# Optimization experiments

Measured on AMD Instinct MI355X. Metric: run time of the kernel, lower is better.

## Reference

```python
import jax, jax.numpy as jnp
import numpy as np

# Config constants (match init_kwargs / config)
B = 16        # config.BATCH_SIZE
T = 2048      # config.TRAIN_LEN
C = 256       # input channels (input_shape[-1])
K = 8         # kernel_size
F = 256       # nb_filters
DIL = 4       # dilation_rate


def setup_inputs() -> dict:
    key = jax.random.key(0)
    k1, k2, k3 = jax.random.split(key, 3)
    inputs = jax.random.normal(k1, (B, T, C), dtype=jnp.float32)
    kernel = jax.random.normal(k2, (C, K, F), dtype=jnp.float32) * 0.05
    bias = jax.random.normal(k3, (F,), dtype=jnp.float32) * 0.05
    return {"inputs": inputs, "kernel": kernel, "bias": bias}


def reference(inputs, kernel, bias):
    # Original TF layer computes, per (b,t,k,f):
    #   raw[b,t,k,f] = sum_c (x[b,t,c] * kernel[c,k,f] + bias[f])
    #               = conv[b,t,k,f] + C * bias[f]
    # (bias is added BEFORE the reduce_sum over the channel axis, so it is
    #  scaled by C — we reproduce that quirk faithfully.)
    # Then each (t,k) slice is scatter-added to output time t + k*dilation
    # (the gather_nd + zero-pad construction in TF implements exactly this
    #  dilated transposed-conv scatter; non-matching positions gather zeros),
    # and finally the last T timesteps are kept.
    Bq, Tq, Cq = inputs.shape
    Kq, Fq = kernel.shape[1], kernel.shape[2]
    conv = jnp.einsum('btc,ckf->btkf', inputs, kernel) + jnp.asarray(Cq, inputs.dtype) * bias
    L = Tq + (Kq - 1) * DIL  # final_time_len
    # scatter positions: out[i + j*DIL] += conv[:, i, j, :]
    pos = (jnp.arange(Tq)[:, None] + DIL * jnp.arange(Kq)[None, :]).reshape(-1)  # (T*K,)
    out = jnp.zeros((Bq, L, Fq), dtype=conv.dtype)
    out = out.at[:, pos, :].add(conv.reshape(Bq, Tq * Kq, Fq))
    return out[:, -Tq:, :]
```

## Files before the change

### kernel.cpp

```cpp
#include <hip/hip_runtime.h>
#include <hip/hip_bf16.h>


#define B_    16
#define T_    2048
#define C_    256
#define KT    8
#define F_    256
#define SH    28
#define BT    64
#define ROWS  (BT + SH)
#define CHW   (ROWS * 64)

typedef __attribute__((ext_vector_type(8))) short short8;
typedef __attribute__((ext_vector_type(4))) float floatx4;

__global__ __launch_bounds__(256) void wprep_kernel(const float* __restrict__ W,
                                                    ushort* __restrict__ Wf) {
    const int tid  = threadIdx.x;
    const int fid  = blockIdx.x * 4 + (tid >> 6);
    const int lane = tid & 63;
    const int g    = fid & 15;
    const int S    = fid >> 4;
    const int kh   = S & 1, j = (S >> 1) & 7, cs = S >> 4;
    const int c0   = cs * 64 + kh * 32 + (lane >> 4) * 8;
    const int f    = g * 16 + (lane & 15);
    short8 pk;
    #pragma unroll
    for (int i = 0; i < 8; ++i) {
        __hip_bfloat16 h = __float2bfloat16(W[((c0 + i) * KT + j) * F_ + f]);
        pk[i] = *reinterpret_cast<const short*>(&h);
    }
    *reinterpret_cast<short8*>(Wf + (size_t)fid * 512 + lane * 8) = pk;
}

__device__ inline short8 cvt8(float4 a, float4 b) {
    float v[8] = {a.x, a.y, a.z, a.w, b.x, b.y, b.z, b.w};
    short8 r;
    #pragma unroll
    for (int i = 0; i < 8; ++i) {
        __hip_bfloat16 h = __float2bfloat16(v[i]);
        r[i] = *reinterpret_cast<const short*>(&h);
    }
    return r;
}

__global__ __launch_bounds__(256, 2) void deconv_kernel(
        const float* __restrict__ x, const ushort* __restrict__ Wf,
        const float* __restrict__ bias, float* __restrict__ out) {
    __shared__ ushort xs[2 * CHW];
    const int t0   = blockIdx.x * BT;
    const int b    = blockIdx.y;
    const int tid  = threadIdx.x;
    const int lane = tid & 63, wf = tid >> 6;
    const int l16  = lane & 15, q = lane >> 4;

    const int r0 = tid >> 3,         g0 = tid & 7;
    const int r1 = (tid + 256) >> 3, g1 = tid & 7;
    const int r2 = (tid + 512) >> 3, g2 = tid & 7;

    float4 A0, B0, A1, B1, A2, B2;

#define STAGE_LOAD(cs_) do {                                                   \
        const float4 z_ = make_float4(0.f, 0.f, 0.f, 0.f);                     \
        A2 = z_; B2 = z_;                                                      \
        {   const float4* p_ = reinterpret_cast<const float4*>(                \
                x + ((size_t)(b * T_ + t0 + r0) * C_ + (cs_) * 64 + g0 * 8));  \
            A0 = p_[0]; B0 = p_[1]; }                                          \
        {   const float4* p_ = reinterpret_cast<const float4*>(                \
                x + ((size_t)(b * T_ + t0 + r1) * C_ + (cs_) * 64 + g1 * 8));  \
            A1 = p_[0]; B1 = p_[1]; }                                          \
        if (tid < 224 && t0 + r2 < T_) {                                       \
            const float4* p_ = reinterpret_cast<const float4*>(                \
                x + ((size_t)(b * T_ + t0 + r2) * C_ + (cs_) * 64 + g2 * 8));  \
            A2 = p_[0]; B2 = p_[1]; } } while (0)

#define STAGE_WRITE(buf_) do {                                                 \
        ushort* d_ = xs + (buf_) * CHW;                                        \
        *reinterpret_cast<short8*>(d_ + r0 * 64 + ((g0 ^ (r0 & 7)) * 8)) =     \
            cvt8(A0, B0);                                                      \
        *reinterpret_cast<short8*>(d_ + r1 * 64 + ((g1 ^ (r1 & 7)) * 8)) =     \
            cvt8(A1, B1);                                                      \
        if (tid < 224)                                                         \
            *reinterpret_cast<short8*>(d_ + r2 * 64 + ((g2 ^ (r2 & 7)) * 8)) = \
                cvt8(A2, B2);                                                  \
        } while (0)

#define LOAD_A(buf_, s_, arr) do {                                             \
        const int j_ = (s_) >> 1, kh_ = (s_) & 1;                              \
        const int rb_ = SH - 4 * j_ + l16;                                     \
        _Pragma("unroll")                                                      \
        for (int mf = 0; mf < 4; ++mf) {                                       \
            const int row_ = rb_ + mf * 16;                                    \
            arr[mf] = *reinterpret_cast<const short8*>(                        \
                xs + (buf_) * CHW + row_ * 64 +                                \
                (((kh_ * 4 + q) ^ (row_ & 7)) * 8));                           \
        } } while (0)

#define LOAD_B(S_, arr) do {                                                   \
        const ushort* p_ = wbase + (size_t)(S_) * 8192;                        \
        _Pragma("unroll")                                                      \
        for (int nf = 0; nf < 4; ++nf)                                         \
            arr[nf] = *reinterpret_cast<const short8*>(p_ + nf * 512);         \
        } while (0)

#define DO_MFMA(aa, bb) do {                                                   \
        _Pragma("unroll")                                                      \
        for (int mf = 0; mf < 4; ++mf)                                         \
            _Pragma("unroll")                                                  \
            for (int nf = 0; nf < 4; ++nf)                                     \
                acc[mf][nf] = __builtin_amdgcn_mfma_f32_16x16x32_bf16(         \
                    aa[mf], bb[nf], acc[mf][nf], 0, 0, 0);                     \
        } while (0)

    const ushort* wbase = Wf + wf * 2048 + (size_t)lane * 8;

    float bf4[4];
    #pragma unroll
    for (int nf = 0; nf < 4; ++nf) bf4[nf] = bias[wf * 64 + nf * 16 + l16];

    floatx4 acc[4][4];
    #pragma unroll
    for (int mf = 0; mf < 4; ++mf)
        #pragma unroll
        for (int nf = 0; nf < 4; ++nf)
            acc[mf][nf] = (floatx4){0.f, 0.f, 0.f, 0.f};

    short8 aA[4], aB[4], bA[4], bB[4];

    STAGE_LOAD(0);
    LOAD_B(0, bA);
    LOAD_B(1, bB);
    STAGE_WRITE(0);
    __syncthreads();

    for (int cs = 0; cs < 4; ++cs) {
        const int buf = cs & 1;
        if (cs < 3) STAGE_LOAD(cs + 1);
        LOAD_A(buf, 0, aA);
        LOAD_A(buf, 1, aB);
        #pragma unroll
        for (int s = 0; s < 16; s += 2) {
            const int S = cs * 16 + s;
            __builtin_amdgcn_s_setprio(1);
            DO_MFMA(aA, bA);
            __builtin_amdgcn_s_setprio(0);
            if (s < 14) LOAD_A(buf, s + 2, aA);
            LOAD_B((S + 2) & 63, bA);
            __builtin_amdgcn_s_setprio(1);
            DO_MFMA(aB, bB);
            __builtin_amdgcn_s_setprio(0);
            if (s < 14) LOAD_A(buf, s + 3, aB);
            LOAD_B((S + 3) & 63, bB);
        }
        if (cs < 3) STAGE_WRITE(buf ^ 1);
        __syncthreads();
    }

    #pragma unroll
    for (int mf = 0; mf < 4; ++mf) {
        #pragma unroll
        for (int nf = 0; nf < 4; ++nf) {
            const int f = wf * 64 + nf * 16 + l16;
            #pragma unroll
            for (int r = 0; r < 4; ++r) {
                const int t = t0 + mf * 16 + q * 4 + r;
                const int jmin = (t < T_ - SH) ? 0 : (((t - (T_ - SH)) >> 2) + 1);
                out[(size_t)(b * T_ + t) * F_ + f] =
                    acc[mf][nf][r] + (float)(8 - jmin) * 256.0f * bf4[nf];
            }
        }
    }
#undef STAGE_LOAD
#undef STAGE_WRITE
#undef LOAD_A
#undef LOAD_B
#undef DO_MFMA
}

extern "C" void kernel_launch(void* const* d_in, const int* in_sizes, int n_in,
                              void* d_out, int out_size, void* d_ws, size_t ws_size,
                              hipStream_t stream) {
    const float* x    = (const float*)d_in[0];
    const float* W    = (const float*)d_in[1];
    const float* bias = (const float*)d_in[2];
    float* out = (float*)d_out;
    ushort* Wf = (ushort*)d_ws;

    wprep_kernel<<<256, 256, 0, stream>>>(W, Wf);
    dim3 grid(T_ / BT, B_);
    deconv_kernel<<<grid, 256, 0, stream>>>(x, Wf, bias, out);
}
```

Before: 44.50 us.

## Retile deconv: 256-row time tiles per block, warps split time, block owns 64 filters

The block tiling changes from 64 time rows × 256 filters (warps split filters) to 256 time rows × 64 filters (warps split time). The channel chunk shrinks to 32, giving 8 stages, and the weight prep layout is reordered to match. Each block now loads only one quarter of the weights, and the shared x tile carries the halo over 256 rows instead of 64, so less redundant x is staged. In exchange the same x tile is reloaded by 4 filter-tile blocks. The number of pipeline iterations and barriers doubles, and the grid keeps 512 blocks.

```diff
diff --git a/kernel.cpp b/kernel.cpp
--- a/kernel.cpp
+++ b/kernel.cpp
@@ -8,9 +8,12 @@
 #define KT    8
 #define F_    256
 #define SH    28
-#define BT    64
+#define BT    256
+#define FW    64
 #define ROWS  (BT + SH)
-#define CHW   (ROWS * 64)
+#define CH    32
+#define CHW   (ROWS * CH)
+#define NTASK (ROWS * 4)
 
 typedef __attribute__((ext_vector_type(8))) short short8;
 typedef __attribute__((ext_vector_type(4))) float floatx4;
@@ -22,8 +25,8 @@
     const int lane = tid & 63;
     const int g    = fid & 15;
     const int S    = fid >> 4;
-    const int kh   = S & 1, j = (S >> 1) & 7, cs = S >> 4;
-    const int c0   = cs * 64 + kh * 32 + (lane >> 4) * 8;
+    const int j    = S & 7, cs = S >> 3;
+    const int c0   = cs * 32 + (lane >> 4) * 8;
     const int f    = g * 16 + (lane & 15);
     short8 pk;
     #pragma unroll
@@ -49,52 +52,50 @@
         const float* __restrict__ x, const ushort* __restrict__ Wf,
         const float* __restrict__ bias, float* __restrict__ out) {
     __shared__ ushort xs[2 * CHW];
-    const int t0   = blockIdx.x * BT;
-    const int b    = blockIdx.y;
+    const int bid  = blockIdx.x;
+    const int ft   = bid >> 7;
+    const int tb   = bid & 127;
+    const int b    = tb >> 3;
+    const int t0   = (tb & 7) * BT;
     const int tid  = threadIdx.x;
-    const int lane = tid & 63, wf = tid >> 6;
+    const int lane = tid & 63, w = tid >> 6;
     const int l16  = lane & 15, q = lane >> 4;
 
-    const int r0 = tid >> 3,         g0 = tid & 7;
-    const int r1 = (tid + 256) >> 3, g1 = tid & 7;
-    const int r2 = (tid + 512) >> 3, g2 = tid & 7;
-
-    float4 A0, B0, A1, B1, A2, B2;
+    float4 SA[5], SB[5];
 
 #define STAGE_LOAD(cs_) do {                                                   \
-        const float4 z_ = make_float4(0.f, 0.f, 0.f, 0.f);                     \
-        A2 = z_; B2 = z_;                                                      \
-        {   const float4* p_ = reinterpret_cast<const float4*>(                \
-                x + ((size_t)(b * T_ + t0 + r0) * C_ + (cs_) * 64 + g0 * 8));  \
-            A0 = p_[0]; B0 = p_[1]; }                                          \
-        {   const float4* p_ = reinterpret_cast<const float4*>(                \
-                x + ((size_t)(b * T_ + t0 + r1) * C_ + (cs_) * 64 + g1 * 8));  \
-            A1 = p_[0]; B1 = p_[1]; }                                          \
-        if (tid < 224 && t0 + r2 < T_) {                                       \
-            const float4* p_ = reinterpret_cast<const float4*>(                \
-                x + ((size_t)(b * T_ + t0 + r2) * C_ + (cs_) * 64 + g2 * 8));  \
-            A2 = p_[0]; B2 = p_[1]; } } while (0)
+        _Pragma("unroll")                                                      \
+        for (int k = 0; k < 5; ++k) {                                          \
+            const int task = tid + k * 256;                                    \
+            const int row_ = task >> 2, g_ = task & 3;                         \
+            SA[k] = make_float4(0.f, 0.f, 0.f, 0.f);                           \
+            SB[k] = make_float4(0.f, 0.f, 0.f, 0.f);                           \
+            if (task < NTASK && t0 + row_ < T_) {                              \
+                const float4* p_ = reinterpret_cast<const float4*>(            \
+                    x + ((size_t)(b * T_ + t0 + row_) * C_ +                   \
+                         (cs_) * CH + g_ * 8));                                \
+                SA[k] = p_[0]; SB[k] = p_[1];                                  \
+            } } } while (0)
 
 #define STAGE_WRITE(buf_) do {                                                 \
         ushort* d_ = xs + (buf_) * CHW;                                        \
-        *reinterpret_cast<short8*>(d_ + r0 * 64 + ((g0 ^ (r0 & 7)) * 8)) =     \
-            cvt8(A0, B0);                                                      \
-        *reinterpret_cast<short8*>(d_ + r1 * 64 + ((g1 ^ (r1 & 7)) * 8)) =     \
-            cvt8(A1, B1);                                                      \
-        if (tid < 224)                                                         \
-            *reinterpret_cast<short8*>(d_ + r2 * 64 + ((g2 ^ (r2 & 7)) * 8)) = \
-                cvt8(A2, B2);                                                  \
-        } while (0)
+        _Pragma("unroll")                                                      \
+        for (int k = 0; k < 5; ++k) {                                          \
+            const int task = tid + k * 256;                                    \
+            const int row_ = task >> 2, g_ = task & 3;                         \
+            if (task < NTASK)                                                  \
+                *reinterpret_cast<short8*>(                                    \
+                    d_ + row_ * CH + ((g_ ^ (row_ & 3)) * 8)) =                \
+                    cvt8(SA[k], SB[k]);                                        \
+        } } while (0)
 
-#define LOAD_A(buf_, s_, arr) do {                                             \
-        const int j_ = (s_) >> 1, kh_ = (s_) & 1;                              \
-        const int rb_ = SH - 4 * j_ + l16;                                     \
+#define LOAD_A(buf_, j_, arr) do {                                             \
+        const int rb_ = SH - 4 * (j_) + w * 64 + l16;                          \
         _Pragma("unroll")                                                      \
         for (int mf = 0; mf < 4; ++mf) {                                       \
             const int row_ = rb_ + mf * 16;                                    \
             arr[mf] = *reinterpret_cast<const short8*>(                        \
-                xs + (buf_) * CHW + row_ * 64 +                                \
-                (((kh_ * 4 + q) ^ (row_ & 7)) * 8));                           \
+                xs + (buf_) * CHW + row_ * CH + ((q ^ (row_ & 3)) * 8));       \
         } } while (0)
 
 #define LOAD_B(S_, arr) do {                                                   \
@@ -113,11 +114,11 @@
                     aa[mf], bb[nf], acc[mf][nf], 0, 0, 0);                     \
         } while (0)
 
-    const ushort* wbase = Wf + wf * 2048 + (size_t)lane * 8;
+    const ushort* wbase = Wf + (size_t)(ft * 4) * 512 + lane * 8;
 
     float bf4[4];
     #pragma unroll
-    for (int nf = 0; nf < 4; ++nf) bf4[nf] = bias[wf * 64 + nf * 16 + l16];
+    for (int nf = 0; nf < 4; ++nf) bf4[nf] = bias[ft * 64 + nf * 16 + l16];
 
     floatx4 acc[4][4];
     #pragma unroll
@@ -134,26 +135,26 @@
     STAGE_WRITE(0);
     __syncthreads();
 
-    for (int cs = 0; cs < 4; ++cs) {
+    for (int cs = 0; cs < 8; ++cs) {
         const int buf = cs & 1;
-        if (cs < 3) STAGE_LOAD(cs + 1);
+        if (cs < 7) STAGE_LOAD(cs + 1);
         LOAD_A(buf, 0, aA);
         LOAD_A(buf, 1, aB);
         #pragma unroll
-        for (int s = 0; s < 16; s += 2) {
-            const int S = cs * 16 + s;
+        for (int j = 0; j < 8; j += 2) {
+            const int S = cs * 8 + j;
             __builtin_amdgcn_s_setprio(1);
             DO_MFMA(aA, bA);
             __builtin_amdgcn_s_setprio(0);
-            if (s < 14) LOAD_A(buf, s + 2, aA);
+            if (j < 6) LOAD_A(buf, j + 2, aA);
             LOAD_B((S + 2) & 63, bA);
             __builtin_amdgcn_s_setprio(1);
             DO_MFMA(aB, bB);
             __builtin_amdgcn_s_setprio(0);
-            if (s < 14) LOAD_A(buf, s + 3, aB);
+            if (j < 6) LOAD_A(buf, j + 3, aB);
             LOAD_B((S + 3) & 63, bB);
         }
-        if (cs < 3) STAGE_WRITE(buf ^ 1);
+        if (cs < 7) STAGE_WRITE(buf ^ 1);
         __syncthreads();
     }
 
@@ -161,10 +162,10 @@
     for (int mf = 0; mf < 4; ++mf) {
         #pragma unroll
         for (int nf = 0; nf < 4; ++nf) {
-            const int f = wf * 64 + nf * 16 + l16;
+            const int f = ft * 64 + nf * 16 + l16;
             #pragma unroll
             for (int r = 0; r < 4; ++r) {
-                const int t = t0 + mf * 16 + q * 4 + r;
+                const int t = t0 + w * 64 + mf * 16 + q * 4 + r;
                 const int jmin = (t < T_ - SH) ? 0 : (((t - (T_ - SH)) >> 2) + 1);
                 out[(size_t)(b * T_ + t) * F_ + f] =
                     acc[mf][nf][r] + (float)(8 - jmin) * 256.0f * bf4[nf];
@@ -188,6 +189,5 @@
     ushort* Wf = (ushort*)d_ws;
 
     wprep_kernel<<<256, 256, 0, stream>>>(W, Wf);
-    dim3 grid(T_ / BT, B_);
-    deconv_kernel<<<grid, 256, 0, stream>>>(x, Wf, bias, out);
+    deconv_kernel<<<512, 256, 0, stream>>>(x, Wf, bias, out);
 }
```

Result: no change. 44.83 us (+0.7%).
